# Kernel tuning notes

Hardware: AMD Instinct MI355X
Metric: run time of the kernel (lower is better)

The kernel has to match this reference:

```python
import jax, jax.numpy as jnp
import numpy as np

B, D, T, H, E = 4, 1024, 2048, 16, 64  # batch, dim, seq_len, n_heads, hidden_dim (H*E == D)


def setup_inputs() -> dict:
    key = jax.random.key(0)
    ks = jax.random.split(key, 6)
    x = jax.random.normal(ks[0], (B, D, T), dtype=jnp.float32)            # (b, e, t) layout
    Wp = jax.random.normal(ks[1], (H, E, D), dtype=jnp.float32) / np.sqrt(D)  # per-head proj weights
    bp = jax.random.normal(ks[2], (H, E), dtype=jnp.float32) * 0.01
    tw = jax.random.normal(ks[3], (H, T), dtype=jnp.float32) / np.sqrt(T)  # per-head Toeplitz kernel, tw[h,0]=diagonal
    Wo = jax.random.normal(ks[4], (D, D), dtype=jnp.float32) / np.sqrt(D)
    bo = jax.random.normal(ks[5], (D,), dtype=jnp.float32) * 0.01
    return {"x": x, "Wp": Wp, "bp": bp, "tw": tw, "Wo": Wo, "bo": bo}


def reference(x, Wp, bp, tw, Wo, bo):
    # x: (b, dim, t) -> (b, t, dim)
    xt = jnp.transpose(x, (0, 2, 1))
    # per-head projections: (b, h, e, t)
    proj = jnp.einsum('btd,hed->bhet', xt, Wp) + bp[None, :, :, None]
    # build per-head causal lower-triangular Toeplitz matrices: Tm[h, t, s] = tw[h, t-s] if s <= t else 0
    idx = jnp.arange(T)[:, None] - jnp.arange(T)[None, :]  # (t, s)
    Tm = jnp.where(idx >= 0, tw[:, jnp.clip(idx, 0)], 0.0)  # (h, t, s)
    # causal Toeplitz mixing along time per head
    mixed = jnp.einsum('hts,bhes->bhet', Tm, proj)          # (b, h, e, t)
    # concat heads on feature dim: (b, t, h*e) == (b, t, dim)
    cat = jnp.transpose(mixed, (0, 3, 1, 2)).reshape(B, T, H * E)
    out = cat @ Wo.T + bo                                   # out_proj: Linear(dim, dim)
    return jnp.transpose(out, (0, 2, 1))                    # back to (b, e, t)
```

## Files before the change

### kernel.cpp

```cpp
#include <hip/hip_runtime.h>
#include <cstdint>

#define NB 4
#define ND 1024
#define NT 2048
#define NH 16
#define NE 64
#define GLEN 2240
#define CAP 2312

typedef __bf16 bf16x8 __attribute__((ext_vector_type(8)));
typedef float f32x4 __attribute__((ext_vector_type(4)));
typedef unsigned short us8 __attribute__((ext_vector_type(8)));
typedef unsigned short us4 __attribute__((ext_vector_type(4)));

__device__ __forceinline__ unsigned short f2bf(float f) {
  unsigned u = __builtin_bit_cast(unsigned, f);
  return (unsigned short)((u + 0x7fffu + ((u >> 16) & 1u)) >> 16);
}

__device__ __forceinline__ void gload16(const void* g, void* l) {
  __builtin_amdgcn_global_load_lds(
      (const __attribute__((address_space(1))) void*)(uintptr_t)g,
      (__attribute__((address_space(3))) void*)(uintptr_t)l, 16, 0, 0);
}

__global__ void prep_kernel(const float* __restrict__ Wp, const float* __restrict__ Wo,
                            const float* __restrict__ tw,
                            unsigned short* __restrict__ WpB, unsigned short* __restrict__ WoB,
                            unsigned short* __restrict__ Gr8) {
  int idx = blockIdx.x * 256 + threadIdx.x;
  int stride = gridDim.x * 256;
  const int n4 = ND * ND / 4;
  for (int i = idx; i < n4; i += stride) {
    float4 v = ((const float4*)Wp)[i];
    us4 o = {f2bf(v.x), f2bf(v.y), f2bf(v.z), f2bf(v.w)};
    ((us4*)WpB)[i] = o;
  }
  for (int i = idx; i < n4; i += stride) {
    float4 v = ((const float4*)Wo)[i];
    us4 o = {f2bf(v.x), f2bf(v.y), f2bf(v.z), f2bf(v.w)};
    ((us4*)WoB)[i] = o;
  }
  for (int i = idx; i < NH * 8 * GLEN; i += stride) {
    int h = i / (8 * GLEN);
    int rem = i - h * 8 * GLEN;
    int r = rem / GLEN;
    int c = rem - r * GLEN;
    int src = c + r;
    Gr8[i] = (src <= NT - 1) ? f2bf(tw[h * NT + (NT - 1) - src]) : (unsigned short)0;
  }
}

__global__ __launch_bounds__(256) void transpose_cast(const float* __restrict__ x,
                                                      unsigned short* __restrict__ xT) {
  __shared__ float tile[64][65];
  const int c = threadIdx.x & 15, r = threadIdx.x >> 4;
  const int t0 = blockIdx.x * 64, d0 = blockIdx.y * 64, b = blockIdx.z;
  const float* xb = x + (long)b * ND * NT;
#pragma unroll
  for (int k = 0; k < 4; ++k) {
    float4 v = *(const float4*)&xb[(long)(d0 + r + 16 * k) * NT + t0 + 4 * c];
    tile[r + 16 * k][4 * c + 0] = v.x;
    tile[r + 16 * k][4 * c + 1] = v.y;
    tile[r + 16 * k][4 * c + 2] = v.z;
    tile[r + 16 * k][4 * c + 3] = v.w;
  }
  __syncthreads();
  unsigned short* xTb = xT + (long)b * NT * ND;
#pragma unroll
  for (int k = 0; k < 4; ++k) {
    int t = r + 16 * k;
    us4 o = {f2bf(tile[4 * c + 0][t]), f2bf(tile[4 * c + 1][t]), f2bf(tile[4 * c + 2][t]),
             f2bf(tile[4 * c + 3][t])};
    *(us4*)&xTb[(long)(t0 + t) * ND + d0 + 4 * c] = o;
  }
}

template <bool OUT_BF16>
__global__ __launch_bounds__(256, 2) void gemm_bt(const unsigned short* __restrict__ A,
                                                  const unsigned short* __restrict__ Bt,
                                                  const float* __restrict__ bias,
                                                  void* __restrict__ Cb, long strideB,
                                                  long strideC) {
  const int N = 2048, K = 1024;
  __shared__ __align__(16) unsigned short As[2][128 * 64];
  __shared__ __align__(16) unsigned short Bs[2][128 * 64];
  const int tid = threadIdx.x;
  const int lane = tid & 63;
  const int wid = tid >> 6;
  const int wm = (wid & 1) * 64, wn = (wid >> 1) * 64;
  const int m0 = blockIdx.y * 128, n0 = blockIdx.x * 128;
  const unsigned short* Bb = Bt + (long)blockIdx.z * strideB;
  const int mlo = lane & 15, q = lane >> 4, m7 = mlo & 7;

  const unsigned short* aP[4];
  const unsigned short* bP[4];
  int dstc[4];
#pragma unroll
  for (int p = 0; p < 4; ++p) {
    int chunk = p * 256 + tid;
    int row = chunk >> 3, blk = chunk & 7;
    int sc = (blk ^ (row & 7)) * 8;
    aP[p] = A + (long)(m0 + row) * K + sc;
    bP[p] = Bb + (long)(n0 + row) * K + sc;
    dstc[p] = chunk * 8;
  }

  auto stage = [&](int buf, int t) {
#pragma unroll
    for (int p = 0; p < 4; ++p) {
      gload16(aP[p] + t * 64, &As[buf][dstc[p]]);
      gload16(bP[p] + t * 64, &Bs[buf][dstc[p]]);
    }
  };

  f32x4 acc[4][4] = {};
  stage(0, 0);

#pragma unroll
  for (int t = 0; t < 16; ++t) {
    const int buf = t & 1;
    asm volatile("s_waitcnt lgkmcnt(0)" ::: "memory");
    __builtin_amdgcn_s_barrier();
    if (t < 15) stage(buf ^ 1, t + 1);
    if (t < 15)
      asm volatile("s_waitcnt vmcnt(8)" ::: "memory");
    else
      asm volatile("s_waitcnt vmcnt(0)" ::: "memory");
    __builtin_amdgcn_s_barrier();
#pragma unroll
    for (int ks = 0; ks < 2; ++ks) {
      bf16x8 av[4], bv[4];
      const int xb8 = ((4 * ks + q) ^ m7) * 8;
#pragma unroll
      for (int i = 0; i < 4; ++i) {
        av[i] = __builtin_bit_cast(bf16x8, *(const us8*)&As[buf][(wm + i * 16 + mlo) * 64 + xb8]);
        bv[i] = __builtin_bit_cast(bf16x8, *(const us8*)&Bs[buf][(wn + i * 16 + mlo) * 64 + xb8]);
      }
      __builtin_amdgcn_s_setprio(1);
#pragma unroll
      for (int i = 0; i < 4; ++i)
#pragma unroll
        for (int j = 0; j < 4; ++j)
          acc[i][j] = __builtin_amdgcn_mfma_f32_16x16x32_bf16(av[i], bv[j], acc[i][j], 0, 0, 0);
      __builtin_amdgcn_s_setprio(0);
    }
  }

#pragma unroll
  for (int i = 0; i < 4; ++i)
#pragma unroll
    for (int j = 0; j < 4; ++j)
#pragma unroll
      for (int r = 0; r < 4; ++r) {
        int gr = m0 + wm + i * 16 + q * 4 + r;
        int gc = n0 + wn + j * 16 + mlo;
        float v = acc[i][j][r] + bias[gr];
        if (OUT_BF16)
          ((unsigned short*)Cb)[(long)blockIdx.z * strideC + (long)gr * N + gc] = f2bf(v);
        else
          ((float*)Cb)[(long)blockIdx.z * strideC + (long)gr * N + gc] = v;
      }
}

__global__ __launch_bounds__(256, 2) void toeplitz(const unsigned short* __restrict__ proj,
                                                   const unsigned short* __restrict__ Gr8,
                                                   unsigned short* __restrict__ mixedT) {
  __shared__ __align__(16) unsigned short Ls[8 * CAP];
  __shared__ __align__(16) unsigned short Bs[4][2][64 * 32];
  const int tid = threadIdx.x, lane = tid & 63, w = tid >> 6;
  const int j = blockIdx.y, h = blockIdx.x, bz = blockIdx.z;
  const int mlo = lane & 15, q = lane >> 4;
  const int wt = (w >> 1) * 64, we = (w & 1) * 32;
  const int t0L = (15 - j) * 128, t0S = j * 128;

  const int delta = (NT - 128) - t0L;
  const int MUSE = t0L + 256;
#pragma unroll 1
  for (int r = 0; r < 8; ++r) {
    int rr = (r + delta) & 7;
    int off8 = r + delta - rr;
    const unsigned short* src = Gr8 + (long)(h * 8 + rr) * GLEN + off8;
    unsigned short* dst = &Ls[r * CAP];
    for (int mc = tid; mc * 8 < MUSE; mc += 256) gload16(src + mc * 8, dst + mc * 8);
  }

  const int rA = (7 - mlo) & 7;
  const int eRow = tid >> 2, kCol = (tid & 3) * 8;
  const unsigned short* bsrc = proj + ((long)bz * ND + h * 64 + eRow) * NT + kCol;

  const int nc0 = 2 * (16 - j);
  const int NCT = 34;
  const unsigned short* lA0 = &Ls[rA * CAP + (127 - wt - mlo - rA) + q * 8];
  const unsigned short* lA1 = lA0 + (t0L - t0S);

  auto stage = [&](int g) {
    int c = (g < nc0) ? g : g - nc0;
    gload16(bsrc + c * 64, &Bs[g & 3][0][tid * 8]);
    gload16(bsrc + c * 64 + 32, &Bs[g & 3][1][tid * 8]);
  };

  stage(0);
  stage(1);
  stage(2);

  f32x4 acc[4][2];
  bf16x8 ap0 = {}, ap1 = {};
  const unsigned short* lA = lA0;

  auto sub = [&](int bf, int hh, int s) {
    bf16x8 a0 = __builtin_bit_cast(bf16x8, *(const us8*)(lA + s));
    bf16x8 a1 = __builtin_bit_cast(bf16x8, *(const us8*)(lA + s - 16));
    bf16x8 b0 = __builtin_bit_cast(bf16x8, *(const us8*)&Bs[bf][hh][(we + mlo) * 32 + q * 8]);
    bf16x8 b1 = __builtin_bit_cast(bf16x8, *(const us8*)&Bs[bf][hh][(we + 16 + mlo) * 32 + q * 8]);
    acc[0][0] = __builtin_amdgcn_mfma_f32_16x16x32_bf16(a0, b0, acc[0][0], 0, 0, 0);
    acc[0][1] = __builtin_amdgcn_mfma_f32_16x16x32_bf16(a0, b1, acc[0][1], 0, 0, 0);
    acc[1][0] = __builtin_amdgcn_mfma_f32_16x16x32_bf16(a1, b0, acc[1][0], 0, 0, 0);
    acc[1][1] = __builtin_amdgcn_mfma_f32_16x16x32_bf16(a1, b1, acc[1][1], 0, 0, 0);
    acc[2][0] = __builtin_amdgcn_mfma_f32_16x16x32_bf16(ap0, b0, acc[2][0], 0, 0, 0);
    acc[2][1] = __builtin_amdgcn_mfma_f32_16x16x32_bf16(ap0, b1, acc[2][1], 0, 0, 0);
    acc[3][0] = __builtin_amdgcn_mfma_f32_16x16x32_bf16(ap1, b0, acc[3][0], 0, 0, 0);
    acc[3][1] = __builtin_amdgcn_mfma_f32_16x16x32_bf16(ap1, b1, acc[3][1], 0, 0, 0);
    ap0 = a0;
    ap1 = a1;
  };

#pragma unroll 1
  for (int g = 0; g < NCT; ++g) {
    if (g + 2 < NCT)
      asm volatile("s_waitcnt vmcnt(4) lgkmcnt(0)" ::: "memory");
    else if (g + 1 < NCT)
      asm volatile("s_waitcnt vmcnt(2) lgkmcnt(0)" ::: "memory");
    else
      asm volatile("s_waitcnt vmcnt(0) lgkmcnt(0)" ::: "memory");
    __builtin_amdgcn_s_barrier();
    if (g + 3 < NCT) stage(g + 3);

    const int pass = (g >= nc0) ? 1 : 0;
    const int c = pass ? g - nc0 : g;
    if (c == 0) {
      lA = pass ? lA1 : lA0;
      ap0 = __builtin_bit_cast(bf16x8, *(const us8*)(lA - 32));
      ap1 = __builtin_bit_cast(bf16x8, *(const us8*)(lA - 48));
#pragma unroll
      for (int i = 0; i < 4; ++i)
#pragma unroll
        for (int jj = 0; jj < 2; ++jj) acc[i][jj] = f32x4{0.f, 0.f, 0.f, 0.f};
    }
    const int buf = g & 3;
    const int s0 = c * 64;
    __builtin_amdgcn_s_setprio(1);
    sub(buf, 0, s0);
    sub(buf, 1, s0 + 32);
    __builtin_amdgcn_s_setprio(0);

    if ((!pass && g == nc0 - 1) || g == NCT - 1) {
      const int t0p = pass ? t0S : t0L;
#pragma unroll
      for (int i = 0; i < 4; ++i)
#pragma unroll
        for (int jj = 0; jj < 2; ++jj)
#pragma unroll
          for (int rr = 0; rr < 4; ++rr) {
            int t = t0p + wt + i * 16 + q * 4 + rr;
            int e = we + jj * 16 + mlo;
            mixedT[((long)bz * NT + t) * ND + h * 64 + e] = f2bf(acc[i][jj][rr]);
          }
    }
  }
}

extern "C" void kernel_launch(void* const* d_in, const int* in_sizes, int n_in, void* d_out,
                              int out_size, void* d_ws, size_t ws_size, hipStream_t stream) {
  const float* x = (const float*)d_in[0];
  const float* Wp = (const float*)d_in[1];
  const float* bp = (const float*)d_in[2];
  const float* tw = (const float*)d_in[3];
  const float* Wo = (const float*)d_in[4];
  const float* bo = (const float*)d_in[5];
  float* out = (float*)d_out;

  char* ws = (char*)d_ws;
  unsigned short* xT = (unsigned short*)(ws);
  unsigned short* proj = (unsigned short*)(ws + (16ull << 20));
  unsigned short* WpB = (unsigned short*)(ws + (32ull << 20));
  unsigned short* WoB = (unsigned short*)(ws + (34ull << 20));
  unsigned short* Gr8 = (unsigned short*)(ws + (36ull << 20));

  prep_kernel<<<dim3(1024), 256, 0, stream>>>(Wp, Wo, tw, WpB, WoB, Gr8);
  transpose_cast<<<dim3(NT / 64, ND / 64, NB), 256, 0, stream>>>(x, xT);
  gemm_bt<true><<<dim3(16, 8, NB), 256, 0, stream>>>(WpB, xT, bp, proj, (long)NT * ND,
                                                     (long)ND * NT);
  toeplitz<<<dim3(NH, 8, NB), 256, 0, stream>>>(proj, Gr8, xT);
  gemm_bt<false><<<dim3(16, 8, NB), 256, 0, stream>>>(WoB, xT, bo, out, (long)NT * ND,
                                                      (long)ND * NT);
}
```

Measured before the change: 155.8 us.

## Load Toeplitz B operands directly from global into registers, drop LDS staging

The Toeplitz kernel stops staging proj tiles through a 4-deep LDS ring with global_load_lds, waitcnt and per-iteration barriers. Each lane now reads its B fragments straight from global memory into registers, prefetching one chunk ahead, and a single __syncthreads follows the Ls load. This removes the per-iteration barriers and the LDS traffic for B and frees 32KB of LDS. The cost is less latency hiding, since only one chunk is in flight, and uncoalesced per-lane 16-byte loads. Two waves that share the same e-columns also read the same data twice.

```diff
diff --git a/kernel.cpp b/kernel.cpp
--- a/kernel.cpp
+++ b/kernel.cpp
@@ -168,7 +168,6 @@
                                                    const unsigned short* __restrict__ Gr8,
                                                    unsigned short* __restrict__ mixedT) {
   __shared__ __align__(16) unsigned short Ls[8 * CAP];
-  __shared__ __align__(16) unsigned short Bs[4][2][64 * 32];
   const int tid = threadIdx.x, lane = tid & 63, w = tid >> 6;
   const int j = blockIdx.y, h = blockIdx.x, bz = blockIdx.z;
   const int mlo = lane & 15, q = lane >> 4;
@@ -185,35 +184,24 @@
     unsigned short* dst = &Ls[r * CAP];
     for (int mc = tid; mc * 8 < MUSE; mc += 256) gload16(src + mc * 8, dst + mc * 8);
   }
+  __syncthreads();
 
   const int rA = (7 - mlo) & 7;
-  const int eRow = tid >> 2, kCol = (tid & 3) * 8;
-  const unsigned short* bsrc = proj + ((long)bz * ND + h * 64 + eRow) * NT + kCol;
-
   const int nc0 = 2 * (16 - j);
   const int NCT = 34;
   const unsigned short* lA0 = &Ls[rA * CAP + (127 - wt - mlo - rA) + q * 8];
   const unsigned short* lA1 = lA0 + (t0L - t0S);
 
-  auto stage = [&](int g) {
-    int c = (g < nc0) ? g : g - nc0;
-    gload16(bsrc + c * 64, &Bs[g & 3][0][tid * 8]);
-    gload16(bsrc + c * 64 + 32, &Bs[g & 3][1][tid * 8]);
-  };
-
-  stage(0);
-  stage(1);
-  stage(2);
+  const unsigned short* bRow0 = proj + ((long)bz * ND + h * 64 + we + mlo) * NT + q * 8;
+  const unsigned short* bRow1 = bRow0 + 16 * (long)NT;
 
   f32x4 acc[4][2];
   bf16x8 ap0 = {}, ap1 = {};
   const unsigned short* lA = lA0;
 
-  auto sub = [&](int bf, int hh, int s) {
+  auto sub = [&](bf16x8 b0, bf16x8 b1, int s) {
     bf16x8 a0 = __builtin_bit_cast(bf16x8, *(const us8*)(lA + s));
     bf16x8 a1 = __builtin_bit_cast(bf16x8, *(const us8*)(lA + s - 16));
-    bf16x8 b0 = __builtin_bit_cast(bf16x8, *(const us8*)&Bs[bf][hh][(we + mlo) * 32 + q * 8]);
-    bf16x8 b1 = __builtin_bit_cast(bf16x8, *(const us8*)&Bs[bf][hh][(we + 16 + mlo) * 32 + q * 8]);
     acc[0][0] = __builtin_amdgcn_mfma_f32_16x16x32_bf16(a0, b0, acc[0][0], 0, 0, 0);
     acc[0][1] = __builtin_amdgcn_mfma_f32_16x16x32_bf16(a0, b1, acc[0][1], 0, 0, 0);
     acc[1][0] = __builtin_amdgcn_mfma_f32_16x16x32_bf16(a1, b0, acc[1][0], 0, 0, 0);
@@ -226,19 +214,23 @@
     ap1 = a1;
   };
 
+  us8 c0 = *(const us8*)(bRow0);
+  us8 c1 = *(const us8*)(bRow1);
+  us8 c2 = *(const us8*)(bRow0 + 32);
+  us8 c3 = *(const us8*)(bRow1 + 32);
+
 #pragma unroll 1
   for (int g = 0; g < NCT; ++g) {
-    if (g + 2 < NCT)
-      asm volatile("s_waitcnt vmcnt(4) lgkmcnt(0)" ::: "memory");
-    else if (g + 1 < NCT)
-      asm volatile("s_waitcnt vmcnt(2) lgkmcnt(0)" ::: "memory");
-    else
-      asm volatile("s_waitcnt vmcnt(0) lgkmcnt(0)" ::: "memory");
-    __builtin_amdgcn_s_barrier();
-    if (g + 3 < NCT) stage(g + 3);
-
     const int pass = (g >= nc0) ? 1 : 0;
     const int c = pass ? g - nc0 : g;
+    us8 n0, n1, n2, n3;
+    if (g + 1 < NCT) {
+      int cN = (g + 1 < nc0) ? g + 1 : g + 1 - nc0;
+      n0 = *(const us8*)(bRow0 + cN * 64);
+      n1 = *(const us8*)(bRow1 + cN * 64);
+      n2 = *(const us8*)(bRow0 + cN * 64 + 32);
+      n3 = *(const us8*)(bRow1 + cN * 64 + 32);
+    }
     if (c == 0) {
       lA = pass ? lA1 : lA0;
       ap0 = __builtin_bit_cast(bf16x8, *(const us8*)(lA - 32));
@@ -248,11 +240,10 @@
 #pragma unroll
         for (int jj = 0; jj < 2; ++jj) acc[i][jj] = f32x4{0.f, 0.f, 0.f, 0.f};
     }
-    const int buf = g & 3;
     const int s0 = c * 64;
     __builtin_amdgcn_s_setprio(1);
-    sub(buf, 0, s0);
-    sub(buf, 1, s0 + 32);
+    sub(__builtin_bit_cast(bf16x8, c0), __builtin_bit_cast(bf16x8, c1), s0);
+    sub(__builtin_bit_cast(bf16x8, c2), __builtin_bit_cast(bf16x8, c3), s0 + 32);
     __builtin_amdgcn_s_setprio(0);
 
     if ((!pass && g == nc0 - 1) || g == NCT - 1) {
@@ -268,6 +259,10 @@
             mixedT[((long)bz * NT + t) * ND + h * 64 + e] = f2bf(acc[i][jj][rr]);
           }
     }
+    c0 = n0;
+    c1 = n1;
+    c2 = n2;
+    c3 = n3;
   }
 }
 
```

Result: slower. 172.6 us (+10.8%).
